# Kernel optimization log

Measured on AMD Instinct MI355X. Metric: run time of the kernel, lower is better.

The kernel has to match this reference:

```python
import jax, jax.numpy as jnp
import numpy as np

B, N, DIM = 4, 2048, 512
HEADS, DIM_HEAD = 8, 64
HID = HEADS * DIM_HEAD


def setup_inputs() -> dict:
    key = jax.random.key(0)
    k1, k2, k3, k4, k5 = jax.random.split(key, 5)
    x = jax.random.normal(k1, (B, N, DIM), jnp.float32)
    pos_bias = jax.random.normal(k2, (HEADS, N, N), jnp.float32) * 0.02
    focus_present_mask = jax.random.bernoulli(k3, 0.5, (B,))
    w_qkv = jax.random.normal(k4, (DIM, 3 * HID), jnp.float32) * (DIM ** -0.5)
    w_out = jax.random.normal(k5, (HID, DIM), jnp.float32) * (HID ** -0.5)
    return {"x": x, "pos_bias": pos_bias, "focus_present_mask": focus_present_mask,
            "w_qkv": w_qkv, "w_out": w_out}


def reference(x, pos_bias, focus_present_mask, w_qkv, w_out):
    scale = DIM_HEAD ** -0.5
    qkv = x @ w_qkv                                   # (B, N, 3*HID)
    q, k, v = jnp.split(qkv, 3, axis=-1)

    def to_heads(t):  # (B, N, HID) -> (B, H, N, D)
        return t.reshape(B, N, HEADS, DIM_HEAD).transpose(0, 2, 1, 3)

    q = to_heads(q) * scale
    k = to_heads(k)
    v = to_heads(v)

    sim = jnp.einsum('bhid,bhjd->bhij', q, k) + pos_bias[None]  # (B, H, N, N)

    # focus_present_mask[b] True -> attend only to self (eye); False -> attend all
    eye = jnp.eye(N, dtype=bool)
    mask = jnp.where(focus_present_mask[:, None, None, None],
                     eye[None, None], jnp.bool_(True))          # (B,1,N,N)
    sim = jnp.where(mask, sim, -jnp.finfo(sim.dtype).max)

    attn = jax.nn.softmax(sim, axis=-1)  # stable softmax == subtract-max + softmax
    out = jnp.einsum('bhij,bhjd->bhid', attn, v)
    out = out.transpose(0, 2, 1, 3).reshape(B, N, HID)
    return out @ w_out
```

## Files before the change

### kernel.cpp

```cpp
#include <hip/hip_runtime.h>
#include <hip/hip_bf16.h>
#include <float.h>

#define B_   4
#define N_   2048
#define DIM_ 512
#define H_   8
#define DH_  64

typedef unsigned short ushort;
typedef __attribute__((ext_vector_type(8))) short short8;
typedef __attribute__((ext_vector_type(4))) float f32x4;

__device__ __forceinline__ ushort f2bf(float f) {
    union { float f; unsigned u; } v; v.f = f;
    return (ushort)((v.u + 0x7fffu + ((v.u >> 16) & 1u)) >> 16);
}
__device__ __forceinline__ float bf2f(ushort u) {
    union { unsigned u; float f; } v; v.u = ((unsigned)u) << 16;
    return v.f;
}

typedef const __attribute__((address_space(1))) unsigned int* gas_t;
typedef __attribute__((address_space(3))) unsigned int* las_t;
__device__ __forceinline__ void gl_lds16(const void* g, void* l) {
    __builtin_amdgcn_global_load_lds((gas_t)g, (las_t)l, 16, 0, 0);
}

__global__ __launch_bounds__(256) void prep_kernel(
    const float* __restrict__ x, const float* __restrict__ wqkv,
    const float* __restrict__ wo,
    ushort* __restrict__ xb, ushort* __restrict__ wqkvT, ushort* __restrict__ woT)
{
    __shared__ ushort tile[64][72];
    const int bx = blockIdx.x;
    const int t = threadIdx.x;
    if (bx < 2048) {
        int gid = bx * 256 + t;
        const float4* xv = (const float4*)x;
        float4 v0 = xv[gid * 2], v1 = xv[gid * 2 + 1];
        uint4 pk;
        pk.x = (unsigned)f2bf(v0.x) | ((unsigned)f2bf(v0.y) << 16);
        pk.y = (unsigned)f2bf(v0.z) | ((unsigned)f2bf(v0.w) << 16);
        pk.z = (unsigned)f2bf(v1.x) | ((unsigned)f2bf(v1.y) << 16);
        pk.w = (unsigned)f2bf(v1.z) | ((unsigned)f2bf(v1.w) << 16);
        ((uint4*)xb)[gid] = pk;
        return;
    }
    int bi = bx - 2048;
    const float* src; ushort* dst; int C, tc, tr;
    if (bi < 192) { src = wqkv; dst = wqkvT; C = 1536; tc = bi % 24; tr = bi / 24; }
    else { bi -= 192; src = wo; dst = woT; C = 512; tc = bi & 7; tr = bi >> 3; }

    const int row = t >> 2, c16 = (t & 3) * 16;
    const float* sp = src + (size_t)(tr * 64 + row) * C + tc * 64 + c16;
    #pragma unroll
    for (int i = 0; i < 4; ++i) {
        float4 v = ((const float4*)sp)[i];
        tile[row][c16 + i * 4 + 0] = f2bf(v.x);
        tile[row][c16 + i * 4 + 1] = f2bf(v.y);
        tile[row][c16 + i * 4 + 2] = f2bf(v.z);
        tile[row][c16 + i * 4 + 3] = f2bf(v.w);
    }
    __syncthreads();
    ushort s[16];
    #pragma unroll
    for (int i = 0; i < 16; ++i) s[i] = tile[c16 + i][row];
    ushort* dp = dst + (size_t)(tc * 64 + row) * 512 + tr * 64 + c16;
    *(uint4*)dp       = *(uint4*)&s[0];
    *(uint4*)(dp + 8) = *(uint4*)&s[8];
}

__global__ __launch_bounds__(256) void vtrans_kernel(
    const ushort* __restrict__ v, ushort* __restrict__ vT)
{
    __shared__ ushort tile[64][72];
    const int nt = blockIdx.x, bh = blockIdx.y;
    const int t = threadIdx.x;
    const int row = t >> 2, c16 = (t & 3) * 16;
    const ushort* src = v + ((size_t)bh * 2048 + nt * 64 + row) * 64 + c16;
    *(uint4*)&tile[row][c16]     = *(const uint4*)src;
    *(uint4*)&tile[row][c16 + 8] = *(const uint4*)(src + 8);
    __syncthreads();
    ushort s[16];
    #pragma unroll
    for (int i = 0; i < 16; ++i) s[i] = tile[c16 + i][row];
    ushort* dst = vT + ((size_t)bh * 64 + row) * 2048 + nt * 64 + c16;
    *(uint4*)dst       = *(uint4*)&s[0];
    *(uint4*)(dst + 8) = *(uint4*)&s[8];
}

__global__ __launch_bounds__(256) void qkv_gemm(
    const ushort* __restrict__ A, const ushort* __restrict__ Bt,
    ushort* __restrict__ qb, ushort* __restrict__ kb, ushort* __restrict__ vb)
{
    __shared__ ushort sA[128 * 64];
    __shared__ ushort sB[128 * 64];
    const int bn = blockIdx.x;
    const int bm = blockIdx.y;
    const int t = threadIdx.x, w_id = t >> 6, lane = t & 63;
    const int l15 = lane & 15, quad = lane >> 4;
    const int mo = (w_id & 1) * 64, no = (w_id >> 1) * 64;
    const int lr = lane >> 3, lc = (lane & 7) * 8;

    f32x4 acc[4][4] = {};

    for (int kt = 0; kt < 8; ++kt) {
        __syncthreads();
        #pragma unroll
        for (int i = 0; i < 4; ++i) {
            int j = w_id * 4 + i;
            gl_lds16(A  + (size_t)(bm * 128 + j * 8 + lr) * 512 + kt * 64 + lc, &sA[j * 512]);
            gl_lds16(Bt + (size_t)(bn * 128 + j * 8 + lr) * 512 + kt * 64 + lc, &sB[j * 512]);
        }
        __syncthreads();
        #pragma unroll
        for (int c = 0; c < 2; ++c) {
            short8 af[4], bf[4];
            #pragma unroll
            for (int mt = 0; mt < 4; ++mt)
                af[mt] = *(const short8*)&sA[(mo + mt * 16 + l15) * 64 + c * 32 + quad * 8];
            #pragma unroll
            for (int n2 = 0; n2 < 4; ++n2)
                bf[n2] = *(const short8*)&sB[(no + n2 * 16 + l15) * 64 + c * 32 + quad * 8];
            #pragma unroll
            for (int mt = 0; mt < 4; ++mt)
                #pragma unroll
                for (int n2 = 0; n2 < 4; ++n2)
                    acc[mt][n2] = __builtin_amdgcn_mfma_f32_16x16x32_bf16(af[mt], bf[n2], acc[mt][n2], 0, 0, 0);
        }
    }

    const int gn0 = bn * 128 + no;
    const int which = gn0 >> 9;
    const int h = (gn0 >> 6) & 7;
    ushort* dst = which == 0 ? qb : (which == 1 ? kb : vb);
    const float sc = which == 0 ? 0.125f : 1.0f;
    #pragma unroll
    for (int mt = 0; mt < 4; ++mt) {
        const int m0 = bm * 128 + mo + mt * 16 + quad * 4;
        #pragma unroll
        for (int n2 = 0; n2 < 4; ++n2) {
            int d = n2 * 16 + l15;
            #pragma unroll
            for (int r = 0; r < 4; ++r) {
                int m = m0 + r, b = m >> 11, n = m & 2047;
                dst[((size_t)(b * 8 + h) * 2048 + n) * 64 + d] = f2bf(acc[mt][n2][r] * sc);
            }
        }
    }
}

__global__ __launch_bounds__(256, 4) void attn_kernel(
    const ushort* __restrict__ qg, const ushort* __restrict__ kg,
    const ushort* __restrict__ vTg, const float* __restrict__ bias,
    const int* __restrict__ mask,
    ushort* __restrict__ po, float* __restrict__ pl)
{
    const int bid = blockIdx.x;
    const int qblk = bid & 31, s = (bid >> 5) & 1, h = (bid >> 6) & 7, b = bid >> 9;
    if (mask[b] != 0) return;

    const int t = threadIdx.x, w_id = t >> 6, lane = t & 63;
    const int l15 = lane & 15, quad = lane >> 4;
    const int lr = lane >> 3;
    const int lcs = ((lane & 7) ^ lr) * 8;
    const int rsw = l15 & 7;
    const int bh = b * 8 + h;
    const int kbase = s * 1024;

    __shared__ ushort lds_k[2][64 * 64];
    __shared__ ushort lds_vt[2][64 * 64];
    __shared__ ushort lds_sp[4 * 16 * 64];

    const ushort* kptr = kg  + (size_t)bh * 2048 * 64;
    const ushort* vtp  = vTg + (size_t)bh * 64 * 2048;

    #pragma unroll
    for (int i = 0; i < 2; ++i) {
        int j = w_id * 2 + i;
        gl_lds16(kptr + (size_t)(kbase + j * 8 + lr) * 64 + lcs, &lds_k[0][j * 512]);
        gl_lds16(vtp + (size_t)(j * 8 + lr) * 2048 + kbase + lcs, &lds_vt[0][j * 512]);
    }

    const ushort* qrp = qg + (size_t)bh * 2048 * 64 + (size_t)(qblk * 64 + w_id * 16 + l15) * 64;
    short8 qf0 = *(const short8*)(qrp + quad * 8);
    short8 qf1 = *(const short8*)(qrp + 32 + quad * 8);

    const int qrow0 = qblk * 64 + w_id * 16 + quad * 4;
    const float* bp = bias + ((size_t)h * 2048 + qrow0) * 2048 + kbase;

    float breg[16];
    #pragma unroll
    for (int tt = 0; tt < 4; ++tt)
        #pragma unroll
        for (int r = 0; r < 4; ++r)
            breg[tt * 4 + r] = bp[(size_t)r * 2048 + tt * 16 + l15];

    f32x4 o[4] = {};
    float lsum[4] = {0.f, 0.f, 0.f, 0.f};

    asm volatile("s_waitcnt vmcnt(0)" ::: "memory");
    __syncthreads();

    for (int it = 0; it < 16; ++it) {
        const int cur = it & 1;
        const ushort* lk = lds_k[cur];
        const ushort* lv = lds_vt[cur];

        if (it + 1 < 16) {
            #pragma unroll
            for (int i = 0; i < 2; ++i) {
                int j = w_id * 2 + i;
                gl_lds16(kptr + (size_t)(kbase + (it + 1) * 64 + j * 8 + lr) * 64 + lcs,
                         &lds_k[cur ^ 1][j * 512]);
                gl_lds16(vtp + (size_t)(j * 8 + lr) * 2048 + kbase + (it + 1) * 64 + lcs,
                         &lds_vt[cur ^ 1][j * 512]);
            }
        }
        __builtin_amdgcn_sched_barrier(0);

        f32x4 sv[4] = {};
        #pragma unroll
        for (int tt = 0; tt < 4; ++tt) {
            const ushort* kr = &lk[(tt * 16 + l15) * 64];
            short8 kf0 = *(const short8*)&kr[(quad ^ rsw) * 8];
            short8 kf1 = *(const short8*)&kr[((4 + quad) ^ rsw) * 8];
            sv[tt] = __builtin_amdgcn_mfma_f32_16x16x32_bf16(qf0, kf0, sv[tt], 0, 0, 0);
            sv[tt] = __builtin_amdgcn_mfma_f32_16x16x32_bf16(qf1, kf1, sv[tt], 0, 0, 0);
        }

        short8 vfa[4], vfb[4];
        #pragma unroll
        for (int nt = 0; nt < 4; ++nt) {
            const ushort* vr = &lv[(nt * 16 + l15) * 64];
            vfa[nt] = *(const short8*)&vr[(quad ^ rsw) * 8];
            vfb[nt] = *(const short8*)&vr[((4 + quad) ^ rsw) * 8];
        }

        #pragma unroll
        for (int tt = 0; tt < 4; ++tt)
            #pragma unroll
            for (int r = 0; r < 4; ++r)
                sv[tt][r] += breg[tt * 4 + r];

        if (it < 15) {
            #pragma unroll
            for (int tt = 0; tt < 4; ++tt)
                #pragma unroll
                for (int r = 0; r < 4; ++r)
                    breg[tt * 4 + r] = bp[(size_t)r * 2048 + (it + 1) * 64 + tt * 16 + l15];
        }

        #pragma unroll
        for (int r = 0; r < 4; ++r) {
            float e0 = __expf(sv[0][r]), e1 = __expf(sv[1][r]);
            float e2 = __expf(sv[2][r]), e3 = __expf(sv[3][r]);
            lsum[r] += (e0 + e1) + (e2 + e3);
            const int prow = w_id * 16 + quad * 4 + r;
            const int prs = prow & 7;
            const int ch = l15 >> 3;
            ushort* pb = &lds_sp[prow * 64 + (l15 & 7)];
            pb[((0 + ch) ^ prs) * 8] = f2bf(e0);
            pb[((2 + ch) ^ prs) * 8] = f2bf(e1);
            pb[((4 + ch) ^ prs) * 8] = f2bf(e2);
            pb[((6 + ch) ^ prs) * 8] = f2bf(e3);
        }

        asm volatile("s_waitcnt lgkmcnt(0)" ::: "memory");
        __builtin_amdgcn_sched_barrier(0);

        const ushort* sp = &lds_sp[(w_id * 16 + l15) * 64];
        short8 pf0 = *(const short8*)&sp[(quad ^ rsw) * 8];
        short8 pf1 = *(const short8*)&sp[((4 + quad) ^ rsw) * 8];
        #pragma unroll
        for (int nt = 0; nt < 4; ++nt) {
            o[nt] = __builtin_amdgcn_mfma_f32_16x16x32_bf16(pf0, vfa[nt], o[nt], 0, 0, 0);
            o[nt] = __builtin_amdgcn_mfma_f32_16x16x32_bf16(pf1, vfb[nt], o[nt], 0, 0, 0);
        }

        asm volatile("s_waitcnt vmcnt(16)" ::: "memory");
        __builtin_amdgcn_s_barrier();
    }

    #pragma unroll
    for (int r = 0; r < 4; ++r) {
        #pragma unroll
        for (int off = 1; off < 16; off <<= 1)
            lsum[r] += __shfl_xor(lsum[r], off, 64);
    }

    #pragma unroll
    for (int r = 0; r < 4; ++r) {
        const int qrow = qrow0 + r;
        const size_t base = ((size_t)(s * 32 + bh) * 2048 + qrow) * 64;
        #pragma unroll
        for (int nt = 0; nt < 4; ++nt)
            po[base + nt * 16 + l15] = f2bf(o[nt][r]);
        if (l15 == 0)
            pl[(size_t)(s * 32 + bh) * 2048 + qrow] = lsum[r];
    }
}

__global__ __launch_bounds__(256) void combine_kernel(
    const ushort* __restrict__ po, const float* __restrict__ pl,
    const ushort* __restrict__ vb, const int* __restrict__ mask,
    ushort* __restrict__ ob)
{
    const int gid = blockIdx.x * 256 + threadIdx.x;
    const int dd = (gid & 7) * 8;
    const int h = (gid >> 3) & 7, n = (gid >> 6) & 2047, b = gid >> 17;
    const int bh = b * 8 + h;
    ushort* op = ob + ((size_t)b * 2048 + n) * 512 + h * 64 + dd;
    if (mask[b] != 0) {
        *(uint4*)op = *(const uint4*)(vb + ((size_t)bh * 2048 + n) * 64 + dd);
        return;
    }
    const size_t i1 = (size_t)bh * 2048 + n;
    const size_t i2 = (size_t)(32 + bh) * 2048 + n;
    float inv = 1.f / (pl[i1] + pl[i2]);
    uint4 ua = *(const uint4*)(po + i1 * 64 + dd);
    uint4 ub = *(const uint4*)(po + i2 * 64 + dd);
    const ushort* pa = (const ushort*)&ua;
    const ushort* pb = (const ushort*)&ub;
    ushort res[8];
    #pragma unroll
    for (int j = 0; j < 8; ++j)
        res[j] = f2bf((bf2f(pa[j]) + bf2f(pb[j])) * inv);
    *(uint4*)op = *(uint4*)res;
}

__global__ __launch_bounds__(256) void out_gemm(
    const ushort* __restrict__ A, const ushort* __restrict__ Bt,
    float* __restrict__ out)
{
    __shared__ ushort sA[2][128 * 64];
    __shared__ ushort sB[2][128 * 64];
    const int bn = blockIdx.x;
    const int bm = blockIdx.y;
    const int t = threadIdx.x, w_id = t >> 6, lane = t & 63;
    const int l15 = lane & 15, quad = lane >> 4;
    const int mo = (w_id & 1) * 64, no = (w_id >> 1) * 64;
    const int lr = lane >> 3;
    const int lcs = ((lane & 7) ^ lr) * 8;
    const int rsw = l15 & 7;

    f32x4 acc[4][4] = {};

    #pragma unroll
    for (int i = 0; i < 4; ++i) {
        int j = w_id * 4 + i;
        gl_lds16(A  + (size_t)(bm * 128 + j * 8 + lr) * 512 + lcs, &sA[0][j * 512]);
        gl_lds16(Bt + (size_t)(bn * 128 + j * 8 + lr) * 512 + lcs, &sB[0][j * 512]);
    }
    asm volatile("s_waitcnt vmcnt(0)" ::: "memory");
    __syncthreads();

    for (int kt = 0; kt < 8; ++kt) {
        const int cur = kt & 1;
        if (kt + 1 < 8) {
            #pragma unroll
            for (int i = 0; i < 4; ++i) {
                int j = w_id * 4 + i;
                gl_lds16(A  + (size_t)(bm * 128 + j * 8 + lr) * 512 + (kt + 1) * 64 + lcs,
                         &sA[cur ^ 1][j * 512]);
                gl_lds16(Bt + (size_t)(bn * 128 + j * 8 + lr) * 512 + (kt + 1) * 64 + lcs,
                         &sB[cur ^ 1][j * 512]);
            }
        }
        #pragma unroll
        for (int c = 0; c < 2; ++c) {
            short8 af[4], bf[4];
            #pragma unroll
            for (int mt = 0; mt < 4; ++mt)
                af[mt] = *(const short8*)&sA[cur][(mo + mt * 16 + l15) * 64 + (((c * 4 + quad) ^ rsw)) * 8];
            #pragma unroll
            for (int n2 = 0; n2 < 4; ++n2)
                bf[n2] = *(const short8*)&sB[cur][(no + n2 * 16 + l15) * 64 + (((c * 4 + quad) ^ rsw)) * 8];
            #pragma unroll
            for (int mt = 0; mt < 4; ++mt)
                #pragma unroll
                for (int n2 = 0; n2 < 4; ++n2)
                    acc[mt][n2] = __builtin_amdgcn_mfma_f32_16x16x32_bf16(af[mt], bf[n2], acc[mt][n2], 0, 0, 0);
        }
        asm volatile("s_waitcnt vmcnt(0)" ::: "memory");
        __syncthreads();
    }
    #pragma unroll
    for (int mt = 0; mt < 4; ++mt) {
        const int m0 = bm * 128 + mo + mt * 16 + quad * 4;
        #pragma unroll
        for (int n2 = 0; n2 < 4; ++n2) {
            int col = bn * 128 + no + n2 * 16 + l15;
            #pragma unroll
            for (int r = 0; r < 4; ++r)
                out[(size_t)(m0 + r) * 512 + col] = acc[mt][n2][r];
        }
    }
}

extern "C" void kernel_launch(void* const* d_in, const int* in_sizes, int n_in,
                              void* d_out, int out_size, void* d_ws, size_t ws_size,
                              hipStream_t stream)
{
    const float* x        = (const float*)d_in[0];
    const float* pos_bias = (const float*)d_in[1];
    const int*   mask     = (const int*)d_in[2];
    const float* w_qkv    = (const float*)d_in[3];
    const float* w_out    = (const float*)d_in[4];
    float* out = (float*)d_out;

    char* ws = (char*)d_ws;
    ushort* qb    = (ushort*)(ws + 0);
    ushort* kb    = (ushort*)(ws + 8388608);
    ushort* vb    = (ushort*)(ws + 16777216);
    ushort* vT    = (ushort*)(ws + 25165824);
    ushort* xb    = (ushort*)(ws + 33554432);
    ushort* ob    = (ushort*)(ws + 33554432);
    ushort* po    = (ushort*)(ws + 41943040);
    float*  pl    = (float* )(ws + 58720256);
    ushort* woT   = (ushort*)(ws + 59244544);
    ushort* wqkvT = (ushort*)(ws + 59768832);

    prep_kernel<<<2304, 256, 0, stream>>>(x, w_qkv, w_out, xb, wqkvT, woT);
    qkv_gemm<<<dim3(12, 64), 256, 0, stream>>>(xb, wqkvT, qb, kb, vb);
    vtrans_kernel<<<dim3(32, 32), 256, 0, stream>>>(vb, vT);
    attn_kernel<<<2048, 256, 0, stream>>>(qb, kb, vT, pos_bias, mask, po, pl);
    combine_kernel<<<2048, 256, 0, stream>>>(po, pl, vb, mask, ob);
    out_gemm<<<dim3(4, 64), 256, 0, stream>>>(ob, woT, out);
}
```

Before: 350.8 us.

## Process unmasked batches in pairs per block to reuse loaded bias tiles

The attention kernel now launches one block per (head, key split, query block) and loops over the unmasked batch entries two at a time, so each pos_bias tile is loaded once and applied to two batches. The aim is to cut the dominant fp32 bias traffic and stop launching blocks that exit early on masked batches. In exchange, the double-buffered K/V prefetch is removed in favour of synchronous loads bracketed by two barriers per iteration, the launch-bounds occupancy hint is dropped, and LDS and register use grow, so load latency is less hidden and fewer blocks may be resident.

```diff
diff --git a/kernel.cpp b/kernel.cpp
--- a/kernel.cpp
+++ b/kernel.cpp
@@ -151,154 +151,202 @@
     }
 }
 
-__global__ __launch_bounds__(256, 4) void attn_kernel(
+__global__ __launch_bounds__(256) void attn_kernel(
     const ushort* __restrict__ qg, const ushort* __restrict__ kg,
     const ushort* __restrict__ vTg, const float* __restrict__ bias,
     const int* __restrict__ mask,
     ushort* __restrict__ po, float* __restrict__ pl)
 {
     const int bid = blockIdx.x;
-    const int qblk = bid & 31, s = (bid >> 5) & 1, h = (bid >> 6) & 7, b = bid >> 9;
-    if (mask[b] != 0) return;
+    const int qblk = bid & 31, s = (bid >> 5) & 1, h = bid >> 6;
+
+    int ub[4]; int nu = 0;
+    #pragma unroll
+    for (int b = 0; b < 4; ++b) if (mask[b] == 0) { ub[nu] = b; ++nu; }
+    if (nu == 0) return;
 
     const int t = threadIdx.x, w_id = t >> 6, lane = t & 63;
     const int l15 = lane & 15, quad = lane >> 4;
     const int lr = lane >> 3;
     const int lcs = ((lane & 7) ^ lr) * 8;
     const int rsw = l15 & 7;
-    const int bh = b * 8 + h;
     const int kbase = s * 1024;
 
-    __shared__ ushort lds_k[2][64 * 64];
-    __shared__ ushort lds_vt[2][64 * 64];
-    __shared__ ushort lds_sp[4 * 16 * 64];
-
-    const ushort* kptr = kg  + (size_t)bh * 2048 * 64;
-    const ushort* vtp  = vTg + (size_t)bh * 64 * 2048;
-
-    #pragma unroll
-    for (int i = 0; i < 2; ++i) {
-        int j = w_id * 2 + i;
-        gl_lds16(kptr + (size_t)(kbase + j * 8 + lr) * 64 + lcs, &lds_k[0][j * 512]);
-        gl_lds16(vtp + (size_t)(j * 8 + lr) * 2048 + kbase + lcs, &lds_vt[0][j * 512]);
-    }
-
-    const ushort* qrp = qg + (size_t)bh * 2048 * 64 + (size_t)(qblk * 64 + w_id * 16 + l15) * 64;
-    short8 qf0 = *(const short8*)(qrp + quad * 8);
-    short8 qf1 = *(const short8*)(qrp + 32 + quad * 8);
+    __shared__ ushort lds_k[2][4096];
+    __shared__ ushort lds_vt[2][4096];
+    __shared__ ushort lds_sp[2][4096];
 
     const int qrow0 = qblk * 64 + w_id * 16 + quad * 4;
     const float* bp = bias + ((size_t)h * 2048 + qrow0) * 2048 + kbase;
 
-    float breg[16];
-    #pragma unroll
-    for (int tt = 0; tt < 4; ++tt)
-        #pragma unroll
-        for (int r = 0; r < 4; ++r)
-            breg[tt * 4 + r] = bp[(size_t)r * 2048 + tt * 16 + l15];
-
-    f32x4 o[4] = {};
-    float lsum[4] = {0.f, 0.f, 0.f, 0.f};
-
-    asm volatile("s_waitcnt vmcnt(0)" ::: "memory");
-    __syncthreads();
-
-    for (int it = 0; it < 16; ++it) {
-        const int cur = it & 1;
-        const ushort* lk = lds_k[cur];
-        const ushort* lv = lds_vt[cur];
-
-        if (it + 1 < 16) {
+    for (int p = 0; p < nu; p += 2) {
+        const int b0 = ub[p];
+        const int has2 = (p + 1 < nu) ? 1 : 0;
+        const int b1 = has2 ? ub[p + 1] : b0;
+        const int bh0 = b0 * 8 + h, bh1 = b1 * 8 + h;
+
+        const ushort* kp0 = kg  + (size_t)bh0 * 2048 * 64;
+        const ushort* vp0 = vTg + (size_t)bh0 * 64 * 2048;
+        const ushort* kp1 = kg  + (size_t)bh1 * 2048 * 64;
+        const ushort* vp1 = vTg + (size_t)bh1 * 64 * 2048;
+
+        const size_t qoff = (size_t)(qblk * 64 + w_id * 16 + l15) * 64;
+        const ushort* q0p = qg + (size_t)bh0 * 2048 * 64 + qoff;
+        const ushort* q1p = qg + (size_t)bh1 * 2048 * 64 + qoff;
+        short8 q0a = *(const short8*)(q0p + quad * 8);
+        short8 q0b = *(const short8*)(q0p + 32 + quad * 8);
+        short8 q1a = *(const short8*)(q1p + quad * 8);
+        short8 q1b = *(const short8*)(q1p + 32 + quad * 8);
+
+        float breg[16];
+        #pragma unroll
+        for (int tt = 0; tt < 4; ++tt)
+            #pragma unroll
+            for (int r = 0; r < 4; ++r)
+                breg[tt * 4 + r] = bp[(size_t)r * 2048 + tt * 16 + l15];
+
+        f32x4 o0[4] = {}, o1[4] = {};
+        float ls0[4] = {0.f, 0.f, 0.f, 0.f};
+        float ls1[4] = {0.f, 0.f, 0.f, 0.f};
+
+        for (int it = 0; it < 16; ++it) {
+            __syncthreads();
             #pragma unroll
             for (int i = 0; i < 2; ++i) {
                 int j = w_id * 2 + i;
-                gl_lds16(kptr + (size_t)(kbase + (it + 1) * 64 + j * 8 + lr) * 64 + lcs,
-                         &lds_k[cur ^ 1][j * 512]);
-                gl_lds16(vtp + (size_t)(j * 8 + lr) * 2048 + kbase + (it + 1) * 64 + lcs,
-                         &lds_vt[cur ^ 1][j * 512]);
-            }
-        }
-        __builtin_amdgcn_sched_barrier(0);
-
-        f32x4 sv[4] = {};
-        #pragma unroll
-        for (int tt = 0; tt < 4; ++tt) {
-            const ushort* kr = &lk[(tt * 16 + l15) * 64];
-            short8 kf0 = *(const short8*)&kr[(quad ^ rsw) * 8];
-            short8 kf1 = *(const short8*)&kr[((4 + quad) ^ rsw) * 8];
-            sv[tt] = __builtin_amdgcn_mfma_f32_16x16x32_bf16(qf0, kf0, sv[tt], 0, 0, 0);
-            sv[tt] = __builtin_amdgcn_mfma_f32_16x16x32_bf16(qf1, kf1, sv[tt], 0, 0, 0);
-        }
-
-        short8 vfa[4], vfb[4];
-        #pragma unroll
-        for (int nt = 0; nt < 4; ++nt) {
-            const ushort* vr = &lv[(nt * 16 + l15) * 64];
-            vfa[nt] = *(const short8*)&vr[(quad ^ rsw) * 8];
-            vfb[nt] = *(const short8*)&vr[((4 + quad) ^ rsw) * 8];
-        }
-
-        #pragma unroll
-        for (int tt = 0; tt < 4; ++tt)
-            #pragma unroll
-            for (int r = 0; r < 4; ++r)
-                sv[tt][r] += breg[tt * 4 + r];
-
-        if (it < 15) {
+                gl_lds16(kp0 + (size_t)(kbase + it * 64 + j * 8 + lr) * 64 + lcs, &lds_k[0][j * 512]);
+                gl_lds16(vp0 + (size_t)(j * 8 + lr) * 2048 + kbase + it * 64 + lcs, &lds_vt[0][j * 512]);
+            }
+            if (has2) {
+                #pragma unroll
+                for (int i = 0; i < 2; ++i) {
+                    int j = w_id * 2 + i;
+                    gl_lds16(kp1 + (size_t)(kbase + it * 64 + j * 8 + lr) * 64 + lcs, &lds_k[1][j * 512]);
+                    gl_lds16(vp1 + (size_t)(j * 8 + lr) * 2048 + kbase + it * 64 + lcs, &lds_vt[1][j * 512]);
+                }
+            }
+            __syncthreads();
+
+            f32x4 sv0[4] = {}, sv1[4] = {};
+            #pragma unroll
+            for (int tt = 0; tt < 4; ++tt) {
+                const ushort* kr = &lds_k[0][(tt * 16 + l15) * 64];
+                short8 kf0 = *(const short8*)&kr[(quad ^ rsw) * 8];
+                short8 kf1 = *(const short8*)&kr[((4 + quad) ^ rsw) * 8];
+                sv0[tt] = __builtin_amdgcn_mfma_f32_16x16x32_bf16(q0a, kf0, sv0[tt], 0, 0, 0);
+                sv0[tt] = __builtin_amdgcn_mfma_f32_16x16x32_bf16(q0b, kf1, sv0[tt], 0, 0, 0);
+            }
+            if (has2) {
+                #pragma unroll
+                for (int tt = 0; tt < 4; ++tt) {
+                    const ushort* kr = &lds_k[1][(tt * 16 + l15) * 64];
+                    short8 kf0 = *(const short8*)&kr[(quad ^ rsw) * 8];
+                    short8 kf1 = *(const short8*)&kr[((4 + quad) ^ rsw) * 8];
+                    sv1[tt] = __builtin_amdgcn_mfma_f32_16x16x32_bf16(q1a, kf0, sv1[tt], 0, 0, 0);
+                    sv1[tt] = __builtin_amdgcn_mfma_f32_16x16x32_bf16(q1b, kf1, sv1[tt], 0, 0, 0);
+                }
+            }
+
             #pragma unroll
             for (int tt = 0; tt < 4; ++tt)
                 #pragma unroll
-                for (int r = 0; r < 4; ++r)
-                    breg[tt * 4 + r] = bp[(size_t)r * 2048 + (it + 1) * 64 + tt * 16 + l15];
+                for (int r = 0; r < 4; ++r) {
+                    sv0[tt][r] += breg[tt * 4 + r];
+                    if (has2) sv1[tt][r] += breg[tt * 4 + r];
+                }
+
+            if (it < 15) {
+                #pragma unroll
+                for (int tt = 0; tt < 4; ++tt)
+                    #pragma unroll
+                    for (int r = 0; r < 4; ++r)
+                        breg[tt * 4 + r] = bp[(size_t)r * 2048 + (it + 1) * 64 + tt * 16 + l15];
+            }
+
+            const int prow = w_id * 16 + quad * 4;
+            const int ch = l15 >> 3;
+            #pragma unroll
+            for (int r = 0; r < 4; ++r) {
+                const int prs = (prow + r) & 7;
+                {
+                    float e0 = __expf(sv0[0][r]), e1 = __expf(sv0[1][r]);
+                    float e2 = __expf(sv0[2][r]), e3 = __expf(sv0[3][r]);
+                    ls0[r] += (e0 + e1) + (e2 + e3);
+                    ushort* pb = &lds_sp[0][(prow + r) * 64 + (l15 & 7)];
+                    pb[((0 + ch) ^ prs) * 8] = f2bf(e0);
+                    pb[((2 + ch) ^ prs) * 8] = f2bf(e1);
+                    pb[((4 + ch) ^ prs) * 8] = f2bf(e2);
+                    pb[((6 + ch) ^ prs) * 8] = f2bf(e3);
+                }
+                if (has2) {
+                    float e0 = __expf(sv1[0][r]), e1 = __expf(sv1[1][r]);
+                    float e2 = __expf(sv1[2][r]), e3 = __expf(sv1[3][r]);
+                    ls1[r] += (e0 + e1) + (e2 + e3);
+                    ushort* pb = &lds_sp[1][(prow + r) * 64 + (l15 & 7)];
+                    pb[((0 + ch) ^ prs) * 8] = f2bf(e0);
+                    pb[((2 + ch) ^ prs) * 8] = f2bf(e1);
+                    pb[((4 + ch) ^ prs) * 8] = f2bf(e2);
+                    pb[((6 + ch) ^ prs) * 8] = f2bf(e3);
+                }
+            }
+
+            asm volatile("s_waitcnt lgkmcnt(0)" ::: "memory");
+
+            {
+                const ushort* sp_ = &lds_sp[0][(w_id * 16 + l15) * 64];
+                short8 pf0 = *(const short8*)&sp_[(quad ^ rsw) * 8];
+                short8 pf1 = *(const short8*)&sp_[((4 + quad) ^ rsw) * 8];
+                #pragma unroll
+                for (int nt = 0; nt < 4; ++nt) {
+                    const ushort* vr = &lds_vt[0][(nt * 16 + l15) * 64];
+                    short8 vf0 = *(const short8*)&vr[(quad ^ rsw) * 8];
+                    short8 vf1 = *(const short8*)&vr[((4 + quad) ^ rsw) * 8];
+                    o0[nt] = __builtin_amdgcn_mfma_f32_16x16x32_bf16(pf0, vf0, o0[nt], 0, 0, 0);
+                    o0[nt] = __builtin_amdgcn_mfma_f32_16x16x32_bf16(pf1, vf1, o0[nt], 0, 0, 0);
+                }
+            }
+            if (has2) {
+                const ushort* sp_ = &lds_sp[1][(w_id * 16 + l15) * 64];
+                short8 pf0 = *(const short8*)&sp_[(quad ^ rsw) * 8];
+                short8 pf1 = *(const short8*)&sp_[((4 + quad) ^ rsw) * 8];
+                #pragma unroll
+                for (int nt = 0; nt < 4; ++nt) {
+                    const ushort* vr = &lds_vt[1][(nt * 16 + l15) * 64];
+                    short8 vf0 = *(const short8*)&vr[(quad ^ rsw) * 8];
+                    short8 vf1 = *(const short8*)&vr[((4 + quad) ^ rsw) * 8];
+                    o1[nt] = __builtin_amdgcn_mfma_f32_16x16x32_bf16(pf0, vf0, o1[nt], 0, 0, 0);
+                    o1[nt] = __builtin_amdgcn_mfma_f32_16x16x32_bf16(pf1, vf1, o1[nt], 0, 0, 0);
+                }
+            }
         }
 
         #pragma unroll
         for (int r = 0; r < 4; ++r) {
-            float e0 = __expf(sv[0][r]), e1 = __expf(sv[1][r]);
-            float e2 = __expf(sv[2][r]), e3 = __expf(sv[3][r]);
-            lsum[r] += (e0 + e1) + (e2 + e3);
-            const int prow = w_id * 16 + quad * 4 + r;
-            const int prs = prow & 7;
-            const int ch = l15 >> 3;
-            ushort* pb = &lds_sp[prow * 64 + (l15 & 7)];
-            pb[((0 + ch) ^ prs) * 8] = f2bf(e0);
-            pb[((2 + ch) ^ prs) * 8] = f2bf(e1);
-            pb[((4 + ch) ^ prs) * 8] = f2bf(e2);
-            pb[((6 + ch) ^ prs) * 8] = f2bf(e3);
-        }
-
-        asm volatile("s_waitcnt lgkmcnt(0)" ::: "memory");
-        __builtin_amdgcn_sched_barrier(0);
-
-        const ushort* sp = &lds_sp[(w_id * 16 + l15) * 64];
-        short8 pf0 = *(const short8*)&sp[(quad ^ rsw) * 8];
-        short8 pf1 = *(const short8*)&sp[((4 + quad) ^ rsw) * 8];
-        #pragma unroll
-        for (int nt = 0; nt < 4; ++nt) {
-            o[nt] = __builtin_amdgcn_mfma_f32_16x16x32_bf16(pf0, vfa[nt], o[nt], 0, 0, 0);
-            o[nt] = __builtin_amdgcn_mfma_f32_16x16x32_bf16(pf1, vfb[nt], o[nt], 0, 0, 0);
-        }
-
-        asm volatile("s_waitcnt vmcnt(16)" ::: "memory");
-        __builtin_amdgcn_s_barrier();
-    }
-
-    #pragma unroll
-    for (int r = 0; r < 4; ++r) {
-        #pragma unroll
-        for (int off = 1; off < 16; off <<= 1)
-            lsum[r] += __shfl_xor(lsum[r], off, 64);
-    }
-
-    #pragma unroll
-    for (int r = 0; r < 4; ++r) {
-        const int qrow = qrow0 + r;
-        const size_t base = ((size_t)(s * 32 + bh) * 2048 + qrow) * 64;
-        #pragma unroll
-        for (int nt = 0; nt < 4; ++nt)
-            po[base + nt * 16 + l15] = f2bf(o[nt][r]);
-        if (l15 == 0)
-            pl[(size_t)(s * 32 + bh) * 2048 + qrow] = lsum[r];
+            #pragma unroll
+            for (int off = 1; off < 16; off <<= 1) {
+                ls0[r] += __shfl_xor(ls0[r], off, 64);
+                ls1[r] += __shfl_xor(ls1[r], off, 64);
+            }
+        }
+
+        #pragma unroll
+        for (int r = 0; r < 4; ++r) {
+            const int qrow = qrow0 + r;
+            const size_t base0 = ((size_t)(s * 32 + bh0) * 2048 + qrow) * 64;
+            #pragma unroll
+            for (int nt = 0; nt < 4; ++nt)
+                po[base0 + nt * 16 + l15] = f2bf(o0[nt][r]);
+            if (l15 == 0)
+                pl[(size_t)(s * 32 + bh0) * 2048 + qrow] = ls0[r];
+            if (has2) {
+                const size_t base1 = ((size_t)(s * 32 + bh1) * 2048 + qrow) * 64;
+                #pragma unroll
+                for (int nt = 0; nt < 4; ++nt)
+                    po[base1 + nt * 16 + l15] = f2bf(o1[nt][r]);
+                if (l15 == 0)
+                    pl[(size_t)(s * 32 + bh1) * 2048 + qrow] = ls1[r];
+            }
+        }
     }
 }
 
@@ -425,7 +473,7 @@
     prep_kernel<<<2304, 256, 0, stream>>>(x, w_qkv, w_out, xb, wqkvT, woT);
     qkv_gemm<<<dim3(12, 64), 256, 0, stream>>>(xb, wqkvT, qb, kb, vb);
     vtrans_kernel<<<dim3(32, 32), 256, 0, stream>>>(vb, vT);
-    attn_kernel<<<2048, 256, 0, stream>>>(qb, kb, vT, pos_bias, mask, po, pl);
+    attn_kernel<<<512, 256, 0, stream>>>(qb, kb, vT, pos_bias, mask, po, pl);
     combine_kernel<<<2048, 256, 0, stream>>>(po, pl, vb, mask, ob);
     out_gemm<<<dim3(4, 64), 256, 0, stream>>>(ob, woT, out);
 }
```

Result: faster. 306.7 us (-12.6%).

## Compact unmasked batches and share pos_bias tile across two batches per block

Applied to the files above, without the earlier changes.

The attention grid is remapped to 1024 blocks, each covering a 32-row query tile for one head and key half. Every block loops over only the unmasked batches, two at a time, with two waves per batch. Both batches reuse the same pos_bias registers, so the bias (the dominant HBM stream) is read once per pair instead of once per batch, and blocks for masked batches are no longer launched as idle. In exchange, the K/V double-buffered prefetch is dropped in favour of synchronous loads with two barriers per iteration. Waves go idle when the count of unmasked batches is odd.

```diff
diff --git a/kernel.cpp b/kernel.cpp
--- a/kernel.cpp
+++ b/kernel.cpp
@@ -157,148 +157,152 @@
     const int* __restrict__ mask,
     ushort* __restrict__ po, float* __restrict__ pl)
 {
-    const int bid = blockIdx.x;
-    const int qblk = bid & 31, s = (bid >> 5) & 1, h = (bid >> 6) & 7, b = bid >> 9;
-    if (mask[b] != 0) return;
+    const int raw  = blockIdx.x;
+    const int work = (raw & 7) * 128 + (raw >> 3);
+    const int qb32 = work & 63, s = (work >> 6) & 1, h = work >> 7;
+
+    int ub[4]; int nu = 0;
+    #pragma unroll
+    for (int b = 0; b < 4; ++b) if (mask[b] == 0) { ub[nu] = b; ++nu; }
+    if (nu == 0) return;
 
     const int t = threadIdx.x, w_id = t >> 6, lane = t & 63;
+    const int wq = w_id & 1;
+    const int wb = w_id >> 1;
     const int l15 = lane & 15, quad = lane >> 4;
     const int lr = lane >> 3;
     const int lcs = ((lane & 7) ^ lr) * 8;
     const int rsw = l15 & 7;
-    const int bh = b * 8 + h;
     const int kbase = s * 1024;
 
-    __shared__ ushort lds_k[2][64 * 64];
-    __shared__ ushort lds_vt[2][64 * 64];
-    __shared__ ushort lds_sp[4 * 16 * 64];
-
-    const ushort* kptr = kg  + (size_t)bh * 2048 * 64;
-    const ushort* vtp  = vTg + (size_t)bh * 64 * 2048;
-
-    #pragma unroll
-    for (int i = 0; i < 2; ++i) {
-        int j = w_id * 2 + i;
-        gl_lds16(kptr + (size_t)(kbase + j * 8 + lr) * 64 + lcs, &lds_k[0][j * 512]);
-        gl_lds16(vtp + (size_t)(j * 8 + lr) * 2048 + kbase + lcs, &lds_vt[0][j * 512]);
-    }
-
-    const ushort* qrp = qg + (size_t)bh * 2048 * 64 + (size_t)(qblk * 64 + w_id * 16 + l15) * 64;
-    short8 qf0 = *(const short8*)(qrp + quad * 8);
-    short8 qf1 = *(const short8*)(qrp + 32 + quad * 8);
-
-    const int qrow0 = qblk * 64 + w_id * 16 + quad * 4;
+    __shared__ ushort lds_k[2][4096];
+    __shared__ ushort lds_vt[2][4096];
+    __shared__ ushort lds_sp[4][1024];
+
+    const int qrow0 = qb32 * 32 + wq * 16 + quad * 4;
     const float* bp = bias + ((size_t)h * 2048 + qrow0) * 2048 + kbase;
 
-    float breg[16];
-    #pragma unroll
-    for (int tt = 0; tt < 4; ++tt)
-        #pragma unroll
-        for (int r = 0; r < 4; ++r)
-            breg[tt * 4 + r] = bp[(size_t)r * 2048 + tt * 16 + l15];
-
-    f32x4 o[4] = {};
-    float lsum[4] = {0.f, 0.f, 0.f, 0.f};
-
-    asm volatile("s_waitcnt vmcnt(0)" ::: "memory");
-    __syncthreads();
-
-    for (int it = 0; it < 16; ++it) {
-        const int cur = it & 1;
-        const ushort* lk = lds_k[cur];
-        const ushort* lv = lds_vt[cur];
-
-        if (it + 1 < 16) {
+    for (int p = 0; p < nu; p += 2) {
+        const int b0 = ub[p];
+        const int has2 = (p + 1 < nu) ? 1 : 0;
+        const int b1 = has2 ? ub[p + 1] : b0;
+        const int bh0 = b0 * 8 + h, bh1 = b1 * 8 + h;
+        const int bhw = wb ? bh1 : bh0;
+        const int active = (wb == 0) || has2;
+
+        const ushort* kp0 = kg  + (size_t)bh0 * 2048 * 64;
+        const ushort* vp0 = vTg + (size_t)bh0 * 64 * 2048;
+        const ushort* kp1 = kg  + (size_t)bh1 * 2048 * 64;
+        const ushort* vp1 = vTg + (size_t)bh1 * 64 * 2048;
+
+        const ushort* qrp = qg + (size_t)bhw * 2048 * 64
+                          + (size_t)(qb32 * 32 + wq * 16 + l15) * 64;
+        short8 qf0 = *(const short8*)(qrp + quad * 8);
+        short8 qf1 = *(const short8*)(qrp + 32 + quad * 8);
+
+        float breg[16];
+        #pragma unroll
+        for (int tt = 0; tt < 4; ++tt)
+            #pragma unroll
+            for (int r = 0; r < 4; ++r)
+                breg[tt * 4 + r] = bp[(size_t)r * 2048 + tt * 16 + l15];
+
+        f32x4 o[4] = {};
+        float lsum[4] = {0.f, 0.f, 0.f, 0.f};
+
+        for (int it = 0; it < 16; ++it) {
+            __syncthreads();
             #pragma unroll
             for (int i = 0; i < 2; ++i) {
                 int j = w_id * 2 + i;
-                gl_lds16(kptr + (size_t)(kbase + (it + 1) * 64 + j * 8 + lr) * 64 + lcs,
-                         &lds_k[cur ^ 1][j * 512]);
-                gl_lds16(vtp + (size_t)(j * 8 + lr) * 2048 + kbase + (it + 1) * 64 + lcs,
-                         &lds_vt[cur ^ 1][j * 512]);
-            }
-        }
-        __builtin_amdgcn_sched_barrier(0);
-
-        f32x4 sv[4] = {};
-        #pragma unroll
-        for (int tt = 0; tt < 4; ++tt) {
-            const ushort* kr = &lk[(tt * 16 + l15) * 64];
-            short8 kf0 = *(const short8*)&kr[(quad ^ rsw) * 8];
-            short8 kf1 = *(const short8*)&kr[((4 + quad) ^ rsw) * 8];
-            sv[tt] = __builtin_amdgcn_mfma_f32_16x16x32_bf16(qf0, kf0, sv[tt], 0, 0, 0);
-            sv[tt] = __builtin_amdgcn_mfma_f32_16x16x32_bf16(qf1, kf1, sv[tt], 0, 0, 0);
-        }
-
-        short8 vfa[4], vfb[4];
-        #pragma unroll
-        for (int nt = 0; nt < 4; ++nt) {
-            const ushort* vr = &lv[(nt * 16 + l15) * 64];
-            vfa[nt] = *(const short8*)&vr[(quad ^ rsw) * 8];
-            vfb[nt] = *(const short8*)&vr[((4 + quad) ^ rsw) * 8];
-        }
-
-        #pragma unroll
-        for (int tt = 0; tt < 4; ++tt)
-            #pragma unroll
-            for (int r = 0; r < 4; ++r)
-                sv[tt][r] += breg[tt * 4 + r];
-
-        if (it < 15) {
-            #pragma unroll
-            for (int tt = 0; tt < 4; ++tt)
-                #pragma unroll
-                for (int r = 0; r < 4; ++r)
-                    breg[tt * 4 + r] = bp[(size_t)r * 2048 + (it + 1) * 64 + tt * 16 + l15];
-        }
-
-        #pragma unroll
-        for (int r = 0; r < 4; ++r) {
-            float e0 = __expf(sv[0][r]), e1 = __expf(sv[1][r]);
-            float e2 = __expf(sv[2][r]), e3 = __expf(sv[3][r]);
-            lsum[r] += (e0 + e1) + (e2 + e3);
-            const int prow = w_id * 16 + quad * 4 + r;
-            const int prs = prow & 7;
-            const int ch = l15 >> 3;
-            ushort* pb = &lds_sp[prow * 64 + (l15 & 7)];
-            pb[((0 + ch) ^ prs) * 8] = f2bf(e0);
-            pb[((2 + ch) ^ prs) * 8] = f2bf(e1);
-            pb[((4 + ch) ^ prs) * 8] = f2bf(e2);
-            pb[((6 + ch) ^ prs) * 8] = f2bf(e3);
-        }
-
-        asm volatile("s_waitcnt lgkmcnt(0)" ::: "memory");
-        __builtin_amdgcn_sched_barrier(0);
-
-        const ushort* sp = &lds_sp[(w_id * 16 + l15) * 64];
-        short8 pf0 = *(const short8*)&sp[(quad ^ rsw) * 8];
-        short8 pf1 = *(const short8*)&sp[((4 + quad) ^ rsw) * 8];
-        #pragma unroll
-        for (int nt = 0; nt < 4; ++nt) {
-            o[nt] = __builtin_amdgcn_mfma_f32_16x16x32_bf16(pf0, vfa[nt], o[nt], 0, 0, 0);
-            o[nt] = __builtin_amdgcn_mfma_f32_16x16x32_bf16(pf1, vfb[nt], o[nt], 0, 0, 0);
-        }
-
-        asm volatile("s_waitcnt vmcnt(16)" ::: "memory");
-        __builtin_amdgcn_s_barrier();
-    }
-
-    #pragma unroll
-    for (int r = 0; r < 4; ++r) {
-        #pragma unroll
-        for (int off = 1; off < 16; off <<= 1)
-            lsum[r] += __shfl_xor(lsum[r], off, 64);
-    }
-
-    #pragma unroll
-    for (int r = 0; r < 4; ++r) {
-        const int qrow = qrow0 + r;
-        const size_t base = ((size_t)(s * 32 + bh) * 2048 + qrow) * 64;
-        #pragma unroll
-        for (int nt = 0; nt < 4; ++nt)
-            po[base + nt * 16 + l15] = f2bf(o[nt][r]);
-        if (l15 == 0)
-            pl[(size_t)(s * 32 + bh) * 2048 + qrow] = lsum[r];
+                gl_lds16(kp0 + (size_t)(kbase + it * 64 + j * 8 + lr) * 64 + lcs, &lds_k[0][j * 512]);
+                gl_lds16(vp0 + (size_t)(j * 8 + lr) * 2048 + kbase + it * 64 + lcs, &lds_vt[0][j * 512]);
+            }
+            if (has2) {
+                #pragma unroll
+                for (int i = 0; i < 2; ++i) {
+                    int j = w_id * 2 + i;
+                    gl_lds16(kp1 + (size_t)(kbase + it * 64 + j * 8 + lr) * 64 + lcs, &lds_k[1][j * 512]);
+                    gl_lds16(vp1 + (size_t)(j * 8 + lr) * 2048 + kbase + it * 64 + lcs, &lds_vt[1][j * 512]);
+                }
+            }
+            __syncthreads();
+
+            if (active) {
+                f32x4 sv[4] = {};
+                #pragma unroll
+                for (int tt = 0; tt < 4; ++tt) {
+                    const ushort* kr = &lds_k[wb][(tt * 16 + l15) * 64];
+                    short8 kf0 = *(const short8*)&kr[(quad ^ rsw) * 8];
+                    short8 kf1 = *(const short8*)&kr[((4 + quad) ^ rsw) * 8];
+                    sv[tt] = __builtin_amdgcn_mfma_f32_16x16x32_bf16(qf0, kf0, sv[tt], 0, 0, 0);
+                    sv[tt] = __builtin_amdgcn_mfma_f32_16x16x32_bf16(qf1, kf1, sv[tt], 0, 0, 0);
+                }
+
+                #pragma unroll
+                for (int tt = 0; tt < 4; ++tt)
+                    #pragma unroll
+                    for (int r = 0; r < 4; ++r)
+                        sv[tt][r] += breg[tt * 4 + r];
+
+                if (it < 15) {
+                    #pragma unroll
+                    for (int tt = 0; tt < 4; ++tt)
+                        #pragma unroll
+                        for (int r = 0; r < 4; ++r)
+                            breg[tt * 4 + r] = bp[(size_t)r * 2048 + (it + 1) * 64 + tt * 16 + l15];
+                }
+
+                const int ch = l15 >> 3;
+                #pragma unroll
+                for (int r = 0; r < 4; ++r) {
+                    const int prow = quad * 4 + r;
+                    const int prs = prow & 7;
+                    float e0 = __expf(sv[0][r]), e1 = __expf(sv[1][r]);
+                    float e2 = __expf(sv[2][r]), e3 = __expf(sv[3][r]);
+                    lsum[r] += (e0 + e1) + (e2 + e3);
+                    ushort* pb = &lds_sp[w_id][prow * 64 + (l15 & 7)];
+                    pb[((0 + ch) ^ prs) * 8] = f2bf(e0);
+                    pb[((2 + ch) ^ prs) * 8] = f2bf(e1);
+                    pb[((4 + ch) ^ prs) * 8] = f2bf(e2);
+                    pb[((6 + ch) ^ prs) * 8] = f2bf(e3);
+                }
+
+                asm volatile("s_waitcnt lgkmcnt(0)" ::: "memory");
+
+                const ushort* sp_ = &lds_sp[w_id][l15 * 64];
+                short8 pf0 = *(const short8*)&sp_[(quad ^ rsw) * 8];
+                short8 pf1 = *(const short8*)&sp_[((4 + quad) ^ rsw) * 8];
+                #pragma unroll
+                for (int nt = 0; nt < 4; ++nt) {
+                    const ushort* vr = &lds_vt[wb][(nt * 16 + l15) * 64];
+                    short8 vf0 = *(const short8*)&vr[(quad ^ rsw) * 8];
+                    short8 vf1 = *(const short8*)&vr[((4 + quad) ^ rsw) * 8];
+                    o[nt] = __builtin_amdgcn_mfma_f32_16x16x32_bf16(pf0, vf0, o[nt], 0, 0, 0);
+                    o[nt] = __builtin_amdgcn_mfma_f32_16x16x32_bf16(pf1, vf1, o[nt], 0, 0, 0);
+                }
+            }
+        }
+
+        if (active) {
+            #pragma unroll
+            for (int r = 0; r < 4; ++r) {
+                #pragma unroll
+                for (int off = 1; off < 16; off <<= 1)
+                    lsum[r] += __shfl_xor(lsum[r], off, 64);
+            }
+
+            #pragma unroll
+            for (int r = 0; r < 4; ++r) {
+                const int qrow = qrow0 + r;
+                const size_t base = ((size_t)(s * 32 + bhw) * 2048 + qrow) * 64;
+                #pragma unroll
+                for (int nt = 0; nt < 4; ++nt)
+                    po[base + nt * 16 + l15] = f2bf(o[nt][r]);
+                if (l15 == 0)
+                    pl[(size_t)(s * 32 + bhw) * 2048 + qrow] = lsum[r];
+            }
+        }
     }
 }
 
@@ -425,7 +429,7 @@
     prep_kernel<<<2304, 256, 0, stream>>>(x, w_qkv, w_out, xb, wqkvT, woT);
     qkv_gemm<<<dim3(12, 64), 256, 0, stream>>>(xb, wqkvT, qb, kb, vb);
     vtrans_kernel<<<dim3(32, 32), 256, 0, stream>>>(vb, vT);
-    attn_kernel<<<2048, 256, 0, stream>>>(qb, kb, vT, pos_bias, mask, po, pl);
+    attn_kernel<<<1024, 256, 0, stream>>>(qb, kb, vT, pos_bias, mask, po, pl);
     combine_kernel<<<2048, 256, 0, stream>>>(po, pl, vb, mask, ob);
     out_gemm<<<dim3(4, 64), 256, 0, stream>>>(ob, woT, out);
 }
```

After: 317.3 us. -9.6%, faster.
